# Kernel optimization log

Hardware: AMD Instinct MI355X
Metric: run time of the kernel (lower is better)

The kernel has to match this reference:

```python
import jax, jax.numpy as jnp
import numpy as np

E4M3_MAX = 448.0  # max representable magnitude of float8_e4m3fn


def setup_inputs() -> dict:
    key = jax.random.key(0)
    k_x, k_w, k_b = jax.random.split(key, 3)
    B, S, K, N = 4, 2048, 4096, 4096  # batch, seq, in_features, out_features
    x = jax.random.normal(k_x, (B, S, K), dtype=jnp.float32)
    # Pre-quantized weight with per-row (per-output-channel) scales, symmetric.
    w_f32 = jax.random.normal(k_w, (N, K), dtype=jnp.float32) * 0.02
    weight_scale = jnp.max(jnp.abs(w_f32), axis=-1) / E4M3_MAX  # [N]
    weight_scale = jnp.maximum(weight_scale, 1e-12)
    weight_fp8 = jnp.clip(w_f32 / weight_scale[:, None], -E4M3_MAX, E4M3_MAX).astype(jnp.float8_e4m3fn)
    bias = jax.random.normal(k_b, (N,), dtype=jnp.float32) * 0.01
    return {"x": x, "weight_fp8": weight_fp8, "weight_scale": weight_scale, "bias": bias}


def reference(x, weight_fp8, weight_scale, bias):
    # x: [B, S, K]; weight_fp8: [N, K] fp8_e4m3; weight_scale: [N]; bias: [N]
    N = weight_fp8.shape[0]
    xr = x.reshape(-1, x.shape[-1])  # [T, K], T = B*S
    # Dynamic per-row (per-token) fp8 quantization of activations.
    amax = jnp.max(jnp.abs(xr), axis=-1, keepdims=True)  # [T, 1]
    in_scale = jnp.maximum(amax / E4M3_MAX, 1e-12).astype(jnp.float32)
    xq = jnp.clip(xr / in_scale, -E4M3_MAX, E4M3_MAX).astype(jnp.float8_e4m3fn)
    # Scaled fp8 GEMM with rowwise dequant scales + bias epilogue.
    acc = jnp.matmul(xq.astype(jnp.float32), weight_fp8.astype(jnp.float32).T)  # [T, N]
    out = acc * in_scale * weight_scale[None, :] + bias[None, :]
    return out.reshape(x.shape[:-1] + (N,))
```

## Files before the change

kernel.cpp:

```cpp
#include <hip/hip_runtime.h>
#include <stdint.h>

#define E4M3_MAX 448.0f
#define E4M3_MIN_SUB 0.001953125f

using f32x4 = __attribute__((ext_vector_type(4))) float;
using ushort8 = __attribute__((ext_vector_type(8))) unsigned short;

__device__ __forceinline__ void gload_lds16(const void* g, void* l) {
  __builtin_amdgcn_global_load_lds(
      (const __attribute__((address_space(1))) void*)g,
      (__attribute__((address_space(3))) void*)l,
      16, 0, 0);
}

__global__ void detect_wfmt(const uint8_t* __restrict__ w, int* __restrict__ flag) {
  __shared__ int cnt[3];
  const int tid = threadIdx.x;
  if (tid < 3) cnt[tid] = 0;
  __syncthreads();
  const uint32_t bits = ((const uint32_t*)w)[tid];
  const float fv = __uint_as_float(bits);
  const float af = fabsf(fv);
  const bool p32 = ((bits & 0xFFFFFu) == 0u) &&
                   (af == 0.f || (af >= E4M3_MIN_SUB && af <= E4M3_MAX));
  bool pbf = true;
#pragma unroll
  for (int h = 0; h < 2; ++h) {
    const uint32_t hb = (bits >> (16 * h)) & 0xFFFFu;
    const float hv = __uint_as_float(hb << 16);
    const float ah = fabsf(hv);
    pbf = pbf && ((hb & 0xFu) == 0u) &&
          (ah == 0.f || (ah >= E4M3_MIN_SUB && ah <= E4M3_MAX));
  }
  const bool pi = bits <= 255u;
  if (p32) atomicAdd(&cnt[0], 1);
  if (pbf) atomicAdd(&cnt[1], 1);
  if (pi) atomicAdd(&cnt[2], 1);
  __syncthreads();
  if (tid == 0) {
    int f;
    if (cnt[0] == 256) f = 0;
    else if (cnt[1] == 256) f = 1;
    else if (cnt[2] == 256) f = 3;
    else f = 2;
    *flag = f;
  }
}

__global__ __launch_bounds__(256) void quant_rows(float* __restrict__ x, int K) {
  const int row = blockIdx.x;
  const int tid = threadIdx.x;
  uint8_t* xrow = (uint8_t*)(x + (size_t)row * K);

  float4 v[4];
  float am = 0.f;
#pragma unroll
  for (int p = 0; p < 4; ++p) {
    v[p] = *(const float4*)((const float*)xrow + p * 1024 + tid * 4);
    am = fmaxf(am, fmaxf(fmaxf(fabsf(v[p].x), fabsf(v[p].y)),
                         fmaxf(fabsf(v[p].z), fabsf(v[p].w))));
  }
#pragma unroll
  for (int off = 32; off > 0; off >>= 1) am = fmaxf(am, __shfl_xor(am, off));
  __shared__ float red[4];
  if ((tid & 63) == 0) red[tid >> 6] = am;
  __syncthreads();
  am = fmaxf(fmaxf(red[0], red[1]), fmaxf(red[2], red[3]));

  const float scale = fmaxf(am / E4M3_MAX, 1e-12f);
  if (tid == 0) *(float*)(xrow + 4096) = scale;

#pragma unroll
  for (int p = 0; p < 4; ++p) {
    float q0 = fminf(fmaxf(v[p].x / scale, -E4M3_MAX), E4M3_MAX);
    float q1 = fminf(fmaxf(v[p].y / scale, -E4M3_MAX), E4M3_MAX);
    float q2 = fminf(fmaxf(v[p].z / scale, -E4M3_MAX), E4M3_MAX);
    float q3 = fminf(fmaxf(v[p].w / scale, -E4M3_MAX), E4M3_MAX);
    int pk = 0;
    pk = __builtin_amdgcn_cvt_pk_fp8_f32(q0, q1, pk, false);
    pk = __builtin_amdgcn_cvt_pk_fp8_f32(q2, q3, pk, true);
    *(int*)(xrow + p * 1024 + tid * 4) = pk;
  }
}

__global__ __launch_bounds__(256) void quant_w(uint8_t* __restrict__ wbase,
                                               const int* __restrict__ flag,
                                               int K) {
  const int f = *flag;
  if (f == 2) return;
  const int row = blockIdx.x;
  const int tid = threadIdx.x;

  if (f == 0) {
    uint8_t* wrow = wbase + (size_t)row * K * 4;
    float4 v[4];
#pragma unroll
    for (int p = 0; p < 4; ++p)
      v[p] = *(const float4*)((const float*)wrow + p * 1024 + tid * 4);
    __syncthreads();
#pragma unroll
    for (int p = 0; p < 4; ++p) {
      float q0 = fminf(fmaxf(v[p].x, -E4M3_MAX), E4M3_MAX);
      float q1 = fminf(fmaxf(v[p].y, -E4M3_MAX), E4M3_MAX);
      float q2 = fminf(fmaxf(v[p].z, -E4M3_MAX), E4M3_MAX);
      float q3 = fminf(fmaxf(v[p].w, -E4M3_MAX), E4M3_MAX);
      int pk = 0;
      pk = __builtin_amdgcn_cvt_pk_fp8_f32(q0, q1, pk, false);
      pk = __builtin_amdgcn_cvt_pk_fp8_f32(q2, q3, pk, true);
      *(int*)(wrow + p * 1024 + tid * 4) = pk;
    }
  } else if (f == 1) {
    uint8_t* wrow = wbase + (size_t)row * K * 2;
#pragma unroll
    for (int p = 0; p < 2; ++p) {
      ushort8 h = *(const ushort8*)((const unsigned short*)wrow + p * 2048 + tid * 8);
      __syncthreads();
      int pk01 = 0, pk23 = 0;
      float q[8];
#pragma unroll
      for (int j = 0; j < 8; ++j) {
        float fv = __uint_as_float(((uint32_t)h[j]) << 16);
        q[j] = fminf(fmaxf(fv, -E4M3_MAX), E4M3_MAX);
      }
      pk01 = __builtin_amdgcn_cvt_pk_fp8_f32(q[0], q[1], pk01, false);
      pk01 = __builtin_amdgcn_cvt_pk_fp8_f32(q[2], q[3], pk01, true);
      pk23 = __builtin_amdgcn_cvt_pk_fp8_f32(q[4], q[5], pk23, false);
      pk23 = __builtin_amdgcn_cvt_pk_fp8_f32(q[6], q[7], pk23, true);
      *(int*)(wrow + p * 2048 + tid * 8) = pk01;
      *(int*)(wrow + p * 2048 + tid * 8 + 4) = pk23;
    }
  } else {
    uint8_t* wrow = wbase + (size_t)row * K * 4;
    int4 v[4];
#pragma unroll
    for (int p = 0; p < 4; ++p)
      v[p] = *(const int4*)((const int*)wrow + p * 1024 + tid * 4);
    __syncthreads();
#pragma unroll
    for (int p = 0; p < 4; ++p) {
      int pk = (v[p].x & 0xFF) | ((v[p].y & 0xFF) << 8) |
               ((v[p].z & 0xFF) << 16) | ((v[p].w & 0xFF) << 24);
      *(int*)(wrow + p * 1024 + tid * 4) = pk;
    }
  }
}

__global__ __launch_bounds__(512, 2) void fp8_gemm(
    const uint8_t* __restrict__ Aq,
    const uint8_t* __restrict__ Wq,
    const int* __restrict__ wflag,
    const float* __restrict__ in_scale,
    const float* __restrict__ w_scale,
    const float* __restrict__ bias,
    float* __restrict__ out,
    int T, int N, int K, int as_bytes, int ss) {
  __shared__ alignas(16) uint8_t S[3][2][2][8192];

  const int tid = threadIdx.x;
  const int w = tid >> 6;
  const int lane = tid & 63;

  const int wf = *wflag;
  const size_t wsb = (wf == 1) ? (size_t)K * 2 : (wf == 2 ? (size_t)K : (size_t)K * 4);

  const int nwg = gridDim.x;
  const int bid = blockIdx.x;
  const int cpx = nwg >> 3;
  const int wg = (bid & 7) * cpx + (bid >> 3);
  const int ntn = N >> 8;
  const int tile_n = (wg % ntn) << 8;
  const int tile_m = (wg / ntn) << 8;

  const int srow = tid >> 1;
  const int sbyte = (tid & 1) << 4;
  const uint8_t* gA = Aq + (size_t)(tile_m + srow) * as_bytes + sbyte;
  const uint8_t* gB = Wq + (size_t)(tile_n + srow) * wsb + sbyte;

  const int wm = w >> 2, wn = w & 3;
  const int fr = lane & 15, fq = lane >> 4;
  const int aoff = (wm * 128 + fr) * 32 + fq * 8;
  const int boff = (wn * 64 + fr) * 32 + fq * 8;

  f32x4 acc[8][4];
#pragma unroll
  for (int i = 0; i < 8; ++i)
#pragma unroll
    for (int j = 0; j < 4; ++j) acc[i][j] = (f32x4){0.f, 0.f, 0.f, 0.f};

#define STAGE(buf_, M_, ks_, k0_)                                        \
  gload_lds16((M_ ? gB : gA) + (k0_) + (ks_) * 32,                       \
              &S[(buf_)][(M_)][(ks_)][w * 1024])

  const int NT = K >> 6;

#pragma unroll
  for (int p = 0; p < 4; ++p) STAGE(0, (p >> 1), (p & 1), 0);
#pragma unroll
  for (int p = 0; p < 4; ++p) STAGE(1, (p >> 1), (p & 1), 64);
  asm volatile("s_waitcnt vmcnt(4)" ::: "memory");
  __builtin_amdgcn_sched_barrier(0);
  __builtin_amdgcn_s_barrier();

  int buf = 0;
  for (int kt = 0; kt < NT; ++kt) {
    const int sbuf = (buf >= 1) ? buf - 1 : buf + 2;
    const int k2 = (kt + 2) << 6;
    const bool pf = (kt + 2) < NT;
    long bfr[4][2];
#pragma unroll
    for (int qd = 0; qd < 4; ++qd) {
      long afr[2][2];
#pragma unroll
      for (int m2 = 0; m2 < 2; ++m2)
#pragma unroll
        for (int ks = 0; ks < 2; ++ks)
          afr[m2][ks] = *(const long*)&S[buf][0][ks][aoff + (qd * 2 + m2) * 512];
      if (qd == 0) {
#pragma unroll
        for (int ni = 0; ni < 4; ++ni)
#pragma unroll
          for (int ks = 0; ks < 2; ++ks)
            bfr[ni][ks] = *(const long*)&S[buf][1][ks][boff + ni * 512];
      }
      if (pf) {
        if (qd == 0) STAGE(sbuf, 0, 0, k2);
        else if (qd == 1) STAGE(sbuf, 0, 1, k2);
        else if (qd == 2) STAGE(sbuf, 1, 0, k2);
        else STAGE(sbuf, 1, 1, k2);
      }
      __builtin_amdgcn_s_barrier();
      __builtin_amdgcn_s_setprio(1);
#pragma unroll
      for (int ks = 0; ks < 2; ++ks)
#pragma unroll
        for (int m2 = 0; m2 < 2; ++m2)
#pragma unroll
          for (int ni = 0; ni < 4; ++ni)
            acc[qd * 2 + m2][ni] = __builtin_amdgcn_mfma_f32_16x16x32_fp8_fp8(
                afr[m2][ks], bfr[ni][ks], acc[qd * 2 + m2][ni], 0, 0, 0);
      __builtin_amdgcn_s_setprio(0);
      if (qd == 3) {
        if (pf) asm volatile("s_waitcnt vmcnt(4)" ::: "memory");
        else    asm volatile("s_waitcnt vmcnt(0)" ::: "memory");
        __builtin_amdgcn_sched_barrier(0);
      }
      __builtin_amdgcn_s_barrier();
    }
    buf = (buf == 2) ? 0 : buf + 1;
  }
#undef STAGE

#pragma unroll
  for (int mi = 0; mi < 8; ++mi) {
    const int r0 = tile_m + wm * 128 + mi * 16 + fq * 4;
    const float s0 = in_scale[(size_t)(r0 + 0) * ss];
    const float s1 = in_scale[(size_t)(r0 + 1) * ss];
    const float s2 = in_scale[(size_t)(r0 + 2) * ss];
    const float s3 = in_scale[(size_t)(r0 + 3) * ss];
#pragma unroll
    for (int ni = 0; ni < 4; ++ni) {
      const int c = tile_n + wn * 64 + ni * 16 + fr;
      const float wsn = w_scale[c];
      const float bn = bias[c];
      float* o = out + (size_t)r0 * N + c;
      o[0]             = acc[mi][ni][0] * s0 * wsn + bn;
      o[(size_t)N]     = acc[mi][ni][1] * s1 * wsn + bn;
      o[(size_t)N * 2] = acc[mi][ni][2] * s2 * wsn + bn;
      o[(size_t)N * 3] = acc[mi][ni][3] * s3 * wsn + bn;
    }
  }
}

extern "C" void kernel_launch(void* const* d_in, const int* in_sizes, int n_in,
                              void* d_out, int out_size, void* d_ws, size_t ws_size,
                              hipStream_t stream) {
  float* x = (float*)d_in[0];
  uint8_t* wq = (uint8_t*)d_in[1];
  const float* wscale = (const float*)d_in[2];
  const float* bias = (const float*)d_in[3];
  float* out = (float*)d_out;
  int* flag = (int*)d_ws;

  const int N = in_sizes[2];
  const int K = in_sizes[1] / N;
  const int T = in_sizes[0] / K;

  detect_wfmt<<<1, 256, 0, stream>>>(wq, flag);
  quant_rows<<<T, 256, 0, stream>>>(x, K);
  quant_w<<<N, 256, 0, stream>>>(wq, flag, K);

  const uint8_t* xq = (const uint8_t*)x;
  const float* in_scale = x + K / 4;
  const int grid = (T / 256) * (N / 256);
  fp8_gemm<<<grid, 512, 0, stream>>>(xq, wq, flag, in_scale, wscale, bias, out,
                                     T, N, K, K * 4, K);
}
```

Before: 529.5 us.

## Repack quantized A and W into tile-contiguous blocks for coalesced GEMM staging

Adds two repack kernels that copy the quantized fp8 activation and weight rows into per-(256-row tile, 64-wide k-slice) contiguous blocks. The blocks go into the unused upper bytes of the fp32 input buffers. The GEMM then streams each stage as contiguous 16-byte chunks and reads LDS fragments with a k-grouped layout, aiming for better global coalescing and fewer LDS bank conflicts. The activation quantizer also multiplies by a reciprocal scale instead of dividing. The trade-off is two extra kernel launches and an additional full read/write pass over both operands.

```diff
diff --git a/kernel.cpp b/kernel.cpp
--- a/kernel.cpp
+++ b/kernel.cpp
@@ -69,14 +69,15 @@
   am = fmaxf(fmaxf(red[0], red[1]), fmaxf(red[2], red[3]));
 
   const float scale = fmaxf(am / E4M3_MAX, 1e-12f);
+  const float rin = 1.0f / scale;
   if (tid == 0) *(float*)(xrow + 4096) = scale;
 
 #pragma unroll
   for (int p = 0; p < 4; ++p) {
-    float q0 = fminf(fmaxf(v[p].x / scale, -E4M3_MAX), E4M3_MAX);
-    float q1 = fminf(fmaxf(v[p].y / scale, -E4M3_MAX), E4M3_MAX);
-    float q2 = fminf(fmaxf(v[p].z / scale, -E4M3_MAX), E4M3_MAX);
-    float q3 = fminf(fmaxf(v[p].w / scale, -E4M3_MAX), E4M3_MAX);
+    float q0 = fminf(fmaxf(v[p].x * rin, -E4M3_MAX), E4M3_MAX);
+    float q1 = fminf(fmaxf(v[p].y * rin, -E4M3_MAX), E4M3_MAX);
+    float q2 = fminf(fmaxf(v[p].z * rin, -E4M3_MAX), E4M3_MAX);
+    float q3 = fminf(fmaxf(v[p].w * rin, -E4M3_MAX), E4M3_MAX);
     int pk = 0;
     pk = __builtin_amdgcn_cvt_pk_fp8_f32(q0, q1, pk, false);
     pk = __builtin_amdgcn_cvt_pk_fp8_f32(q2, q3, pk, true);
@@ -146,6 +147,53 @@
   }
 }
 
+__global__ __launch_bounds__(256) void repack_A(uint8_t* __restrict__ xb, int K) {
+  const int nkt = K >> 6;
+  const int g = blockIdx.x / nkt;
+  const int kt = blockIdx.x % nkt;
+  const int lr = threadIdx.x;
+  const size_t rowb = (size_t)K * 4;
+  const uint8_t* s = xb + (size_t)(g * 256 + lr) * rowb + kt * 64;
+  uint4 d0 = *(const uint4*)(s);
+  uint4 d1 = *(const uint4*)(s + 16);
+  uint4 d2 = *(const uint4*)(s + 32);
+  uint4 d3 = *(const uint4*)(s + 48);
+  uint2 pc[8] = {{d0.x, d0.y}, {d0.z, d0.w}, {d1.x, d1.y}, {d1.z, d1.w},
+                 {d2.x, d2.y}, {d2.z, d2.w}, {d3.x, d3.y}, {d3.z, d3.w}};
+  const size_t p = (size_t)g * nkt + kt;
+#pragma unroll
+  for (int pi = 0; pi < 8; ++pi)
+    *(uint2*)(xb + (2 * p + (pi >> 2)) * 16384 + 8192 + (pi & 3) * 2048 + lr * 8) = pc[pi];
+}
+
+__global__ __launch_bounds__(256) void repack_W(uint8_t* __restrict__ wb,
+                                                const int* __restrict__ flag,
+                                                int K) {
+  const int f = *flag;
+  if (f == 2) return;
+  const int nkt = K >> 6;
+  const int g = blockIdx.x / nkt;
+  const int kt = blockIdx.x % nkt;
+  const int lr = threadIdx.x;
+  const size_t rowb = (f == 1) ? (size_t)K * 2 : (size_t)K * 4;
+  const uint8_t* s = wb + (size_t)(g * 256 + lr) * rowb + kt * 64;
+  uint4 d0 = *(const uint4*)(s);
+  uint4 d1 = *(const uint4*)(s + 16);
+  uint4 d2 = *(const uint4*)(s + 32);
+  uint4 d3 = *(const uint4*)(s + 48);
+  uint2 pc[8] = {{d0.x, d0.y}, {d0.z, d0.w}, {d1.x, d1.y}, {d1.z, d1.w},
+                 {d2.x, d2.y}, {d2.z, d2.w}, {d3.x, d3.y}, {d3.z, d3.w}};
+  const size_t p = (size_t)g * nkt + kt;
+#pragma unroll
+  for (int pi = 0; pi < 8; ++pi) {
+    const int pb = (pi >> 2) * 8192 + (pi & 3) * 2048 + lr * 8;
+    uint8_t* d;
+    if (f == 1) d = wb + (4 * p + (pb >> 12)) * 8192 + 4096 + (pb & 4095);
+    else        d = wb + (2 * p + (pi >> 2)) * 16384 + 8192 + (pb & 8191);
+    *(uint2*)d = pc[pi];
+  }
+}
+
 __global__ __launch_bounds__(512, 2) void fp8_gemm(
     const uint8_t* __restrict__ Aq,
     const uint8_t* __restrict__ Wq,
@@ -154,15 +202,14 @@
     const float* __restrict__ w_scale,
     const float* __restrict__ bias,
     float* __restrict__ out,
-    int T, int N, int K, int as_bytes, int ss) {
+    int T, int N, int K, int ss) {
   __shared__ alignas(16) uint8_t S[3][2][2][8192];
 
   const int tid = threadIdx.x;
   const int w = tid >> 6;
   const int lane = tid & 63;
-
   const int wf = *wflag;
-  const size_t wsb = (wf == 1) ? (size_t)K * 2 : (wf == 2 ? (size_t)K : (size_t)K * 4);
+  const int nkt = K >> 6;
 
   const int nwg = gridDim.x;
   const int bid = blockIdx.x;
@@ -171,16 +218,20 @@
   const int ntn = N >> 8;
   const int tile_n = (wg % ntn) << 8;
   const int tile_m = (wg / ntn) << 8;
-
-  const int srow = tid >> 1;
-  const int sbyte = (tid & 1) << 4;
-  const uint8_t* gA = Aq + (size_t)(tile_m + srow) * as_bytes + sbyte;
-  const uint8_t* gB = Wq + (size_t)(tile_n + srow) * wsb + sbyte;
+  const int gm = tile_m >> 8, gn = tile_n >> 8;
+
+  const uint8_t* aS = Aq + (size_t)2 * gm * nkt * 16384 + 8192 + tid * 16;
+  const uint8_t* bS0 = Wq + (size_t)2 * gn * nkt * 16384 + 8192 + tid * 16;
+  const uint8_t* bS1 = Wq + ((size_t)4 * gn * nkt + (tid >> 8)) * 8192 + 4096 +
+                       ((tid * 16) & 4095);
+  const uint8_t* bS2 = Wq + (size_t)(tile_n + (tid >> 1)) * K + ((tid & 1) << 4);
 
   const int wm = w >> 2, wn = w & 3;
   const int fr = lane & 15, fq = lane >> 4;
-  const int aoff = (wm * 128 + fr) * 32 + fq * 8;
-  const int boff = (wn * 64 + fr) * 32 + fq * 8;
+  const int a_base = fq * 2048 + (wm * 128 + fr) * 8;
+  const int b_base = (wf == 2) ? ((wn * 64 + fr) * 32 + fq * 8)
+                               : (fq * 2048 + (wn * 64 + fr) * 8);
+  const int b_step = (wf == 2) ? 512 : 128;
 
   f32x4 acc[8][4];
 #pragma unroll
@@ -188,16 +239,17 @@
 #pragma unroll
     for (int j = 0; j < 4; ++j) acc[i][j] = (f32x4){0.f, 0.f, 0.f, 0.f};
 
-#define STAGE(buf_, M_, ks_, k0_)                                        \
-  gload_lds16((M_ ? gB : gA) + (k0_) + (ks_) * 32,                       \
-              &S[(buf_)][(M_)][(ks_)][w * 1024])
-
-  const int NT = K >> 6;
-
-#pragma unroll
-  for (int p = 0; p < 4; ++p) STAGE(0, (p >> 1), (p & 1), 0);
-#pragma unroll
-  for (int p = 0; p < 4; ++p) STAGE(1, (p >> 1), (p & 1), 64);
+#define STAGE_A(buf_, ks_, kt_)                                              \
+  gload_lds16(aS + (size_t)(2 * (kt_) + (ks_)) * 16384, &S[(buf_)][0][(ks_)][w * 1024])
+#define STAGE_B(buf_, ks_, kt_)                                              \
+  gload_lds16((wf == 2) ? (bS2 + (kt_) * 64 + (ks_) * 32)                    \
+              : (wf == 1) ? (bS1 + (size_t)(4 * (kt_) + 2 * (ks_)) * 8192)   \
+                          : (bS0 + (size_t)(2 * (kt_) + (ks_)) * 16384),     \
+              &S[(buf_)][1][(ks_)][w * 1024])
+
+  const int NT = nkt;
+  STAGE_A(0, 0, 0); STAGE_A(0, 1, 0); STAGE_B(0, 0, 0); STAGE_B(0, 1, 0);
+  STAGE_A(1, 0, 1); STAGE_A(1, 1, 1); STAGE_B(1, 0, 1); STAGE_B(1, 1, 1);
   asm volatile("s_waitcnt vmcnt(4)" ::: "memory");
   __builtin_amdgcn_sched_barrier(0);
   __builtin_amdgcn_s_barrier();
@@ -205,8 +257,8 @@
   int buf = 0;
   for (int kt = 0; kt < NT; ++kt) {
     const int sbuf = (buf >= 1) ? buf - 1 : buf + 2;
-    const int k2 = (kt + 2) << 6;
-    const bool pf = (kt + 2) < NT;
+    const int k2 = kt + 2;
+    const bool pf = k2 < NT;
     long bfr[4][2];
 #pragma unroll
     for (int qd = 0; qd < 4; ++qd) {
@@ -215,19 +267,19 @@
       for (int m2 = 0; m2 < 2; ++m2)
 #pragma unroll
         for (int ks = 0; ks < 2; ++ks)
-          afr[m2][ks] = *(const long*)&S[buf][0][ks][aoff + (qd * 2 + m2) * 512];
+          afr[m2][ks] = *(const long*)&S[buf][0][ks][a_base + (qd * 2 + m2) * 128];
       if (qd == 0) {
 #pragma unroll
         for (int ni = 0; ni < 4; ++ni)
 #pragma unroll
           for (int ks = 0; ks < 2; ++ks)
-            bfr[ni][ks] = *(const long*)&S[buf][1][ks][boff + ni * 512];
+            bfr[ni][ks] = *(const long*)&S[buf][1][ks][b_base + ni * b_step];
       }
       if (pf) {
-        if (qd == 0) STAGE(sbuf, 0, 0, k2);
-        else if (qd == 1) STAGE(sbuf, 0, 1, k2);
-        else if (qd == 2) STAGE(sbuf, 1, 0, k2);
-        else STAGE(sbuf, 1, 1, k2);
+        if (qd == 0) STAGE_A(sbuf, 0, k2);
+        else if (qd == 1) STAGE_A(sbuf, 1, k2);
+        else if (qd == 2) STAGE_B(sbuf, 0, k2);
+        else STAGE_B(sbuf, 1, k2);
       }
       __builtin_amdgcn_s_barrier();
       __builtin_amdgcn_s_setprio(1);
@@ -249,7 +301,8 @@
     }
     buf = (buf == 2) ? 0 : buf + 1;
   }
-#undef STAGE
+#undef STAGE_A
+#undef STAGE_B
 
 #pragma unroll
   for (int mi = 0; mi < 8; ++mi) {
@@ -289,10 +342,11 @@
   detect_wfmt<<<1, 256, 0, stream>>>(wq, flag);
   quant_rows<<<T, 256, 0, stream>>>(x, K);
   quant_w<<<N, 256, 0, stream>>>(wq, flag, K);
-
-  const uint8_t* xq = (const uint8_t*)x;
+  repack_A<<<(T / 256) * (K / 64), 256, 0, stream>>>((uint8_t*)x, K);
+  repack_W<<<(N / 256) * (K / 64), 256, 0, stream>>>(wq, flag, K);
+
   const float* in_scale = x + K / 4;
   const int grid = (T / 256) * (N / 256);
-  fp8_gemm<<<grid, 512, 0, stream>>>(xq, wq, flag, in_scale, wscale, bias, out,
-                                     T, N, K, K * 4, K);
-}
+  fp8_gemm<<<grid, 512, 0, stream>>>((const uint8_t*)x, wq, flag, in_scale,
+                                     wscale, bias, out, T, N, K, K);
+}
```

After: 498.6 us. 1.06x faster.
